# Kernel optimization log

Hardware: AMD Instinct MI355X
Metric: run time of the kernel (lower is better)

Reference implementation:

```python
import jax, jax.numpy as jnp
import numpy as np

B, S, D, H = 1, 4096, 1024, 16
HD = D // H  # head_size = 64

def setup_inputs() -> dict:
    key = jax.random.key(0)
    ks = jax.random.split(key, 9)
    scale = 1.0 / np.sqrt(D)
    return {
        "x": jax.random.normal(ks[0], (B, S, D), jnp.float32),
        "Wq": jax.random.normal(ks[1], (D, D), jnp.float32) * scale,
        "bq": jax.random.normal(ks[2], (D,), jnp.float32) * 0.01,
        "Wk": jax.random.normal(ks[3], (D, D), jnp.float32) * scale,
        "bk": jax.random.normal(ks[4], (D,), jnp.float32) * 0.01,
        "Wv": jax.random.normal(ks[5], (D, D), jnp.float32) * scale,
        "bv": jax.random.normal(ks[6], (D,), jnp.float32) * 0.01,
        "Wo": jax.random.normal(ks[7], (D, D), jnp.float32) * scale,
        "bo": jax.random.normal(ks[8], (D,), jnp.float32) * 0.01,
    }

def _split_heads(t):
    # (B, S, D) -> (B, H, S, HD)
    return t.reshape(B, S, H, HD).transpose(0, 2, 1, 3)

def reference(x, Wq, bq, Wk, bk, Wv, bv, Wo, bo):
    q = _split_heads(x @ Wq + bq)
    k = _split_heads(x @ Wk + bk)
    v = _split_heads(x @ Wv + bv)
    # scores: (B, H, S, S), materialized as in the original naive attention
    scores = jnp.einsum('bhqd,bhkd->bhqk', q, k) / jnp.sqrt(jnp.asarray(HD, q.dtype))
    causal = jnp.tril(jnp.ones((S, S), dtype=bool))  # tril mask, broadcast over (B, H)
    scores = jnp.where(causal[None, None], scores, jnp.asarray(-1e9, scores.dtype))
    attn = jax.nn.softmax(scores, axis=-1)
    out = jnp.einsum('bhqk,bhkd->bhqd', attn, v)  # (B, H, S, HD)
    out = out.transpose(0, 2, 1, 3).reshape(B, S, D)  # combine heads
    return out @ Wo + bo
```

## Files before the change

kernel.cpp:

```cpp
#include <hip/hip_runtime.h>

#define SEQ 4096
#define DM  1024
#define NH  16
#define HDIM 64

typedef unsigned short u16;
typedef unsigned int   u32;
typedef __bf16 bf16x8 __attribute__((ext_vector_type(8)));
typedef float f32x4 __attribute__((ext_vector_type(4)));

__device__ __forceinline__ float bf2f(u16 u) {
    unsigned v = ((unsigned)u) << 16;
    float f;
    __builtin_memcpy(&f, &v, 4);
    return f;
}
__device__ __forceinline__ u16 f2bf(float f) {
    unsigned u;
    __builtin_memcpy(&u, &f, 4);
    return (u16)((u + 0x7fffu + ((u >> 16) & 1u)) >> 16);
}
__device__ __forceinline__ u32 bfpack(float a, float b) {
    u32 ua, ub;
    __builtin_memcpy(&ua, &a, 4);
    __builtin_memcpy(&ub, &b, 4);
    return ((ua + 0x8000u) >> 16) | ((ub + 0x8000u) & 0xffff0000u);
}

typedef const __attribute__((address_space(1))) unsigned int gas_uint;
typedef __attribute__((address_space(3))) unsigned int las_uint;
__device__ __forceinline__ void gld16(const u16* g, u16* l) {
    __builtin_amdgcn_global_load_lds((gas_uint*)g, (las_uint*)l, 16, 0, 0);
}

__device__ __forceinline__ f32x4 mfma16(bf16x8 a, bf16x8 b, f32x4 c) {
    return __builtin_amdgcn_mfma_f32_16x16x32_bf16(a, b, c, 0, 0, 0);
}

#define QSCALE 0.18033688011f

__global__ __launch_bounds__(256) void detect_k(const u16* __restrict__ w,
                                                int* __restrict__ flags) {
    __shared__ float red[256];
    const int t = threadIdx.x;
    float mx = 0.f;
    for (int i = t; i < 4096; i += 256) {
        float v = fabsf(bf2f(w[i]));
        if (v < 3e38f) mx = fmaxf(mx, v);
    }
    red[t] = mx;
    __syncthreads();
    for (int s = 128; s > 0; s >>= 1) {
        if (t < s) red[t] = fmaxf(red[t], red[t + s]);
        __syncthreads();
    }
    if (t == 0) {
        flags[0] = (red[0] > 1e4f) ? 1 : 0;
        flags[1] = 0;
    }
}

__global__ __launch_bounds__(256) void prep_w(const void* w0, const void* w1,
                                              const void* w2, const void* w3,
                                              const void* b0, const void* b1,
                                              const void* b2, const void* b3,
                                              u16* __restrict__ wt,
                                              u16* __restrict__ b_dst,
                                              const int* __restrict__ flags) {
    __shared__ u16 tile[32][33];
    const int f = flags[0];
    const int z = blockIdx.z;
    const void* win[4] = {w0, w1, w2, w3};
    const void* bin[4] = {b0, b1, b2, b3};
    const void* in = win[z];
    u16* out = wt + (size_t)z * DM * DM;
    const float scale = (z == 0) ? QSCALE : 1.0f;

    const int bx = blockIdx.x * 32;
    const int by = blockIdx.y * 32;
    const int tx = threadIdx.x & 31;
    const int ty = threadIdx.x >> 5;
#pragma unroll
    for (int i = ty; i < 32; i += 8) {
        size_t idx = (size_t)(by + i) * DM + bx + tx;
        float v = f ? ((const float*)in)[idx] : bf2f(((const u16*)in)[idx]);
        tile[i][tx] = f2bf(v * scale);
    }
    __syncthreads();
#pragma unroll
    for (int i = ty; i < 32; i += 8) out[(size_t)(bx + i) * DM + by + tx] = tile[tx][i];

    if (blockIdx.x == 0 && blockIdx.y == 0) {
        const void* bi = bin[z];
        for (int i = threadIdx.x; i < DM; i += 256) {
            float v = f ? ((const float*)bi)[i] : bf2f(((const u16*)bi)[i]);
            b_dst[z * DM + i] = f2bf(v * scale);
        }
    }
}

__global__ __launch_bounds__(256) void cvt_x8(const void* __restrict__ src,
                                              u16* __restrict__ dst,
                                              const int* __restrict__ flags) {
    const size_t i = ((size_t)blockIdx.x * 256 + threadIdx.x) * 8;
    if (flags[0]) {
        const float4* s4 = (const float4*)((const float*)src + i);
        float4 a = s4[0], b = s4[1];
        uint4 o;
        o.x = bfpack(a.x, a.y);
        o.y = bfpack(a.z, a.w);
        o.z = bfpack(b.x, b.y);
        o.w = bfpack(b.z, b.w);
        *(uint4*)(dst + i) = o;
    } else {
        *(uint4*)(dst + i) = *(const uint4*)((const u16*)src + i);
    }
}

__global__ __launch_bounds__(256, 2) void gemm128(const u16* __restrict__ A,
                                                  const u16* __restrict__ Bt,
                                                  const u16* __restrict__ bias,
                                                  void* __restrict__ C0,
                                                  void* __restrict__ C1,
                                                  void* __restrict__ C2,
                                                  int M, int N, int K,
                                                  const int* __restrict__ flags) {
    __shared__ u16 As[128 * 32];
    __shared__ u16 Bs[128 * 32];
    const int f    = flags[0];
    const int tid  = threadIdx.x;
    const int lane = tid & 63;
    const int w    = tid >> 6;
    const int m    = lane & 15;
    const int quad = lane >> 4;
    const int wr   = w >> 1;
    const int wc   = w & 1;
    const int mb = blockIdx.x * 128;
    const int nb = blockIdx.y * 128;
    const int mat = nb >> 10;
    const int lnb = nb & 1023;
    void* C = (mat == 0) ? C0 : ((mat == 1) ? C1 : C2);

    f32x4 acc[4][4] = {};

    for (int kb = 0; kb < K; kb += 32) {
        __syncthreads();
#pragma unroll
        for (int i = 0; i < 2; ++i) {
            const int Lb = i * 256 + w * 64;
            const int L  = Lb + lane;
            const int row = L >> 2, cb = L & 3;
            gld16(&A[(size_t)(mb + row) * K + kb + cb * 8], &As[Lb * 8]);
            gld16(&Bt[(size_t)(nb + row) * K + kb + cb * 8], &Bs[Lb * 8]);
        }
        __syncthreads();

        bf16x8 af[4];
#pragma unroll
        for (int mt = 0; mt < 4; ++mt)
            af[mt] = *(const bf16x8*)&As[(wr * 64 + mt * 16 + m) * 32 + quad * 8];
#pragma unroll
        for (int ct = 0; ct < 4; ++ct) {
            bf16x8 bfr = *(const bf16x8*)&Bs[(wc * 64 + ct * 16 + m) * 32 + quad * 8];
#pragma unroll
            for (int mt = 0; mt < 4; ++mt)
                acc[mt][ct] = mfma16(af[mt], bfr, acc[mt][ct]);
        }
    }

#pragma unroll
    for (int ct = 0; ct < 4; ++ct) {
        float bv = bf2f(bias[nb + wc * 64 + ct * 16 + m]);
#pragma unroll
        for (int mt = 0; mt < 4; ++mt) {
#pragma unroll
            for (int r = 0; r < 4; ++r) {
                int row = mb + wr * 64 + mt * 16 + quad * 4 + r;
                size_t idx = (size_t)row * DM + lnb + wc * 64 + ct * 16 + m;
                float v = acc[mt][ct][r] + bv;
                if (f) ((float*)C)[idx] = v;
                else   ((u16*)C)[idx]   = f2bf(v);
            }
        }
    }
}

__global__ __launch_bounds__(256, 2) void gemm_n64(const u16* __restrict__ A,
                                                   const u16* __restrict__ Bt,
                                                   const u16* __restrict__ bias,
                                                   void* __restrict__ C,
                                                   int M, int N, int K,
                                                   const int* __restrict__ flags) {
    __shared__ u16 As[128 * 32];
    __shared__ u16 Bs[64 * 32];
    const int f    = flags[0];
    const int tid  = threadIdx.x;
    const int lane = tid & 63;
    const int w    = tid >> 6;
    const int m    = lane & 15;
    const int quad = lane >> 4;
    const int mb = blockIdx.x * 128;
    const int nb = blockIdx.y * 64;

    f32x4 acc[2][4] = {};

    for (int kb = 0; kb < K; kb += 32) {
        __syncthreads();
#pragma unroll
        for (int i = 0; i < 2; ++i) {
            const int Lb = (2 * w + i) * 64;
            const int L  = Lb + lane;
            const int row = L >> 2, cb = L & 3;
            gld16(&A[(size_t)(mb + row) * K + kb + cb * 8], &As[Lb * 8]);
        }
        {
            const int L = w * 64 + lane;
            const int row = L >> 2, cb = L & 3;
            gld16(&Bt[(size_t)(nb + row) * K + kb + cb * 8], &Bs[w * 512]);
        }
        __syncthreads();

        bf16x8 af[2];
#pragma unroll
        for (int mt = 0; mt < 2; ++mt)
            af[mt] = *(const bf16x8*)&As[(w * 32 + mt * 16 + m) * 32 + quad * 8];
#pragma unroll
        for (int ct = 0; ct < 4; ++ct) {
            bf16x8 bfr = *(const bf16x8*)&Bs[(ct * 16 + m) * 32 + quad * 8];
#pragma unroll
            for (int mt = 0; mt < 2; ++mt)
                acc[mt][ct] = mfma16(af[mt], bfr, acc[mt][ct]);
        }
    }

#pragma unroll
    for (int ct = 0; ct < 4; ++ct) {
        float bv = bf2f(bias[nb + ct * 16 + m]);
#pragma unroll
        for (int mt = 0; mt < 2; ++mt) {
#pragma unroll
            for (int r = 0; r < 4; ++r) {
                int row = mb + w * 32 + mt * 16 + quad * 4 + r;
                size_t idx = (size_t)row * N + nb + ct * 16 + m;
                float v = acc[mt][ct][r] + bv;
                if (f) ((float*)C)[idx] = v;
                else   ((u16*)C)[idx]   = f2bf(v);
            }
        }
    }
}

__global__ __launch_bounds__(256) void vt_k(const u16* __restrict__ V,
                                            u16* __restrict__ Vt) {
    __shared__ u16 T[64][72];
    const int st = blockIdx.x;
    const int h  = blockIdx.y;
    const int t  = threadIdx.x;
    const int sl = t >> 2, c = t & 3;
    const u16* src = &V[(size_t)(st * 64 + sl) * DM + h * 64 + c * 16];
    *(uint4*)&T[sl][c * 16]     = *(const uint4*)src;
    *(uint4*)&T[sl][c * 16 + 8] = *(const uint4*)(src + 8);
    __syncthreads();
    const int dl = t >> 2, c2 = t & 3;
    u16 tmp[16];
#pragma unroll
    for (int i = 0; i < 16; ++i) tmp[i] = T[c2 * 16 + i][dl];
    u16* dst = &Vt[(size_t)(h * 64 + dl) * SEQ + st * 64 + c2 * 16];
    *(uint4*)dst       = *(const uint4*)&tmp[0];
    *(uint4*)(dst + 8) = *(const uint4*)&tmp[8];
}

__global__ __launch_bounds__(256, 2) void attn_split(const u16* __restrict__ Qb,
                                                     const u16* __restrict__ Kb,
                                                     const u16* __restrict__ Vt,
                                                     u16* __restrict__ slot0,
                                                     u16* __restrict__ slot1,
                                                     u16* __restrict__ slot2,
                                                     float* __restrict__ l0,
                                                     float* __restrict__ l1,
                                                     float* __restrict__ l2) {
    __shared__ u16 Ks[2][128 * 64];
    __shared__ u16 Vs[2][64 * 128];

    const int tid  = threadIdx.x;
    const int lane = tid & 63;
    const int w    = tid >> 6;
    const int m    = lane & 15;
    const int quad = lane >> 4;
    const int l3   = lane >> 3;
    const int l4   = lane >> 4;
    const int m7   = m & 7;
    const int cxk  = ((lane & 7) ^ l3) * 8;

    const int b    = blockIdx.x;
    const int x    = b & 7;
    const int u    = b >> 3;
    const int qt2  = 15 - (u / 6);
    const int v6   = u % 6;
    const int head = 2 * x + (v6 / 3);
    const int part = v6 % 3;
    const int hc   = head * HDIM;
    const int n128 = 2 * qt2 + 2;
    const int k0t  = part * n128 / 3;
    const int k1t  = (part + 1) * n128 / 3 - 1;

    const int qw = qt2 * 256 + w * 64;
    const int dw = qw >> 6;

    bf16x8 qf[4][2];
#pragma unroll
    for (int qt4 = 0; qt4 < 4; ++qt4)
#pragma unroll
        for (int c = 0; c < 2; ++c)
            qf[qt4][c] = *(const bf16x8*)&Qb[(size_t)(qw + qt4 * 16 + m) * DM + hc + c * 32 + quad * 8];

    f32x4 o_acc[4][4] = {};
    float l_part[4] = {0.f, 0.f, 0.f, 0.f};

#pragma unroll
    for (int i = 0; i < 4; ++i) {
        const int kr = w * 32 + i * 8 + l3;
        gld16(&Kb[(size_t)(k0t * 128 + kr) * DM + hc + cxk], &Ks[0][(w * 32 + i * 8) * 64]);
        const int vr = w * 16 + i * 4 + l4;
        const int cxv = ((lane & 15) ^ ((i * 4 + l4) & 7)) * 8;
        gld16(&Vt[(size_t)(hc + vr) * SEQ + k0t * 128 + cxv], &Vs[0][(w * 16 + i * 4) * 128]);
    }

    for (int kt = k0t; kt <= k1t; ++kt) {
        const int cur = (kt - k0t) & 1;
        __syncthreads();

        if (kt < k1t) {
            const int nbf = 1 - cur;
            const int nkt = kt + 1;
#pragma unroll
            for (int i = 0; i < 4; ++i) {
                const int kr = w * 32 + i * 8 + l3;
                gld16(&Kb[(size_t)(nkt * 128 + kr) * DM + hc + cxk], &Ks[nbf][(w * 32 + i * 8) * 64]);
                const int vr = w * 16 + i * 4 + l4;
                const int cxv = ((lane & 15) ^ ((i * 4 + l4) & 7)) * 8;
                gld16(&Vt[(size_t)(hc + vr) * SEQ + nkt * 128 + cxv], &Vs[nbf][(w * 16 + i * 4) * 128]);
            }
        }

        const u16* ksb = Ks[cur];
        const u16* vsb = Vs[cur];

#pragma unroll
        for (int h = 0; h < 2; ++h) {
            const int t64 = kt * 2 + h;
            if (t64 > dw) continue;

#pragma unroll
            for (int p = 0; p < 2; ++p) {
                const int ph = 2 * h + p;
                uint4 pa_raw[4];

#pragma unroll
                for (int stt = 0; stt < 2; ++stt) {
                    const int st = ph * 2 + stt;
                    bf16x8 kf[2];
#pragma unroll
                    for (int c = 0; c < 2; ++c)
                        kf[c] = *(const bf16x8*)&ksb[(st * 16 + m) * 64 + (((c * 4 + quad) ^ m7) * 8)];

                    f32x4 sc[4];
#pragma unroll
                    for (int qt4 = 0; qt4 < 4; ++qt4) {
                        f32x4 a = {};
                        a = mfma16(kf[0], qf[qt4][0], a);
                        a = mfma16(kf[1], qf[qt4][1], a);
                        sc[qt4] = a;
                    }

                    if (t64 == dw) {
                        const int stl = 2 * p + stt;
#pragma unroll
                        for (int qt4 = 0; qt4 < 4; ++qt4)
#pragma unroll
                            for (int r = 0; r < 4; ++r) {
                                float pp = __builtin_amdgcn_exp2f(sc[qt4][r]);
                                sc[qt4][r] = (stl * 16 + quad * 4 + r > qt4 * 16 + m) ? 0.f : pp;
                            }
                    } else {
#pragma unroll
                        for (int qt4 = 0; qt4 < 4; ++qt4)
#pragma unroll
                            for (int r = 0; r < 4; ++r)
                                sc[qt4][r] = __builtin_amdgcn_exp2f(sc[qt4][r]);
                    }

#pragma unroll
                    for (int qt4 = 0; qt4 < 4; ++qt4) {
                        l_part[qt4] += sc[qt4][0] + sc[qt4][1] + sc[qt4][2] + sc[qt4][3];
                        const u32 pk0 = bfpack(sc[qt4][0], sc[qt4][1]);
                        const u32 pk1 = bfpack(sc[qt4][2], sc[qt4][3]);
                        if (stt == 0) { pa_raw[qt4].x = pk0; pa_raw[qt4].y = pk1; }
                        else          { pa_raw[qt4].z = pk0; pa_raw[qt4].w = pk1; }
                    }
                }

                bf16x8 pa[4];
#pragma unroll
                for (int qt4 = 0; qt4 < 4; ++qt4) __builtin_memcpy(&pa[qt4], &pa_raw[qt4], 16);

#pragma unroll
                for (int dt = 0; dt < 4; ++dt) {
                    const int base = (dt * 16 + m) * 128;
                    const int clo = ((4 * ph + (quad >> 1)) ^ m7) * 8 + (quad & 1) * 4;
                    const int chi = ((4 * ph + 2 + (quad >> 1)) ^ m7) * 8 + (quad & 1) * 4;
                    uint2 vlo = *(const uint2*)&vsb[base + clo];
                    uint2 vhi = *(const uint2*)&vsb[base + chi];
                    uint4 t;
                    t.x = vlo.x; t.y = vlo.y; t.z = vhi.x; t.w = vhi.y;
                    bf16x8 vf;
                    __builtin_memcpy(&vf, &t, 16);
#pragma unroll
                    for (int qt4 = 0; qt4 < 4; ++qt4)
                        o_acc[qt4][dt] = mfma16(pa[qt4], vf, o_acc[qt4][dt]);
                }
            }
        }
    }

#pragma unroll
    for (int qt4 = 0; qt4 < 4; ++qt4) {
        l_part[qt4] += __shfl_xor(l_part[qt4], 16, 64);
        l_part[qt4] += __shfl_xor(l_part[qt4], 32, 64);
    }

    u16*   dst = (part == 0) ? slot0 : ((part == 1) ? slot1 : slot2);
    float* lb  = (part == 0) ? l0 : ((part == 1) ? l1 : l2);
#pragma unroll
    for (int qt4 = 0; qt4 < 4; ++qt4)
#pragma unroll
        for (int dt = 0; dt < 4; ++dt)
#pragma unroll
            for (int r = 0; r < 4; ++r) {
                int row = qw + qt4 * 16 + quad * 4 + r;
                dst[(size_t)row * DM + hc + dt * 16 + m] = f2bf(o_acc[qt4][dt][r]);
            }
    if (lane < 16) {
#pragma unroll
        for (int qt4 = 0; qt4 < 4; ++qt4)
            lb[head * SEQ + qw + qt4 * 16 + lane] = l_part[qt4];
    }
}

__global__ __launch_bounds__(256) void merge_k(u16* __restrict__ s0,
                                               const u16* __restrict__ s1,
                                               const u16* __restrict__ s2,
                                               const float* __restrict__ l0,
                                               const float* __restrict__ l1,
                                               const float* __restrict__ l2) {
    const int gid = blockIdx.x * 256 + threadIdx.x;
    const int rl = gid >> 7;
    const int cg = gid & 127;
    const int h  = cg >> 3;
    const float inv = 1.0f / (l0[h * SEQ + rl] + l1[h * SEQ + rl] + l2[h * SEQ + rl]);
    uint4 va = *(const uint4*)(s0 + (size_t)rl * DM + cg * 8);
    uint4 vb = *(const uint4*)(s1 + (size_t)rl * DM + cg * 8);
    uint4 vc = *(const uint4*)(s2 + (size_t)rl * DM + cg * 8);
    const u16* a16 = (const u16*)&va;
    const u16* b16 = (const u16*)&vb;
    const u16* c16 = (const u16*)&vc;
    u16 oo[8];
#pragma unroll
    for (int i = 0; i < 8; ++i)
        oo[i] = f2bf((bf2f(a16[i]) + bf2f(b16[i]) + bf2f(c16[i])) * inv);
    *(uint4*)(s0 + (size_t)rl * DM + cg * 8) = *(const uint4*)&oo[0];
}

extern "C" void kernel_launch(void* const* d_in, const int* in_sizes, int n_in,
                              void* d_out, int out_size, void* d_ws, size_t ws_size,
                              hipStream_t stream) {
    (void)in_sizes; (void)n_in; (void)out_size; (void)ws_size;

    u16* ws    = (u16*)d_ws;
    int* flags = (int*)d_ws;
    u16* xc    = ws + 64;
    u16* Vt_g  = xc;
    u16* Wtqkv = xc + (size_t)SEQ * DM;
    u16* Wto   = Wtqkv + (size_t)3 * DM * DM;
    u16* bqkv  = Wto + (size_t)DM * DM;
    u16* boc   = bqkv + 3 * DM;
    u16* Qb    = boc + DM;
    u16* Kb    = Qb + (size_t)SEQ * DM;
    u16* Vb    = Kb + (size_t)SEQ * DM;
    u16* ab    = Vb + (size_t)SEQ * DM;
    u16* slotB = ab + (size_t)SEQ * DM;
    u16* slotC = Vb;
    float* l0f = (float*)Wtqkv;
    float* l1f = l0f + NH * SEQ;
    float* l2f = l1f + NH * SEQ;

    detect_k<<<1, 256, 0, stream>>>((const u16*)d_in[1], flags);

    prep_w<<<dim3(DM / 32, DM / 32, 4), 256, 0, stream>>>(
        d_in[1], d_in[3], d_in[5], d_in[7],
        d_in[2], d_in[4], d_in[6], d_in[8],
        Wtqkv, bqkv, flags);

    cvt_x8<<<SEQ * DM / 2048, 256, 0, stream>>>(d_in[0], xc, flags);

    gemm128<<<dim3(SEQ / 128, 3 * DM / 128), 256, 0, stream>>>(
        xc, Wtqkv, bqkv, Qb, Kb, Vb, SEQ, 3 * DM, DM, flags + 1);

    vt_k<<<dim3(SEQ / 64, NH), 256, 0, stream>>>(Vb, Vt_g);

    attn_split<<<dim3(768), 256, 0, stream>>>(Qb, Kb, Vt_g, ab, slotB, slotC,
                                              l0f, l1f, l2f);

    merge_k<<<dim3(SEQ * 128 / 256), 256, 0, stream>>>(ab, slotB, slotC, l0f, l1f, l2f);

    gemm_n64<<<dim3(SEQ / 128, DM / 64), 256, 0, stream>>>(
        ab, Wto, boc, d_out, SEQ, DM, DM, flags);
}
```

Baseline: 220.5 us.

## Fuse prep kernels, write V transposed from QKV GEMM, remap GEMM block order

Merges the dtype-detect, weight transpose and x conversion kernels into one launch, with each block doing its own dtype check. The QKV GEMM now writes V directly in transposed layout, so the separate transpose kernel and its round trip through global memory go away. Both GEMMs switch to a 1D grid with a remapped block order, likely aiming for better L2 reuse of the weight tiles. This cuts launch count and memory traffic, but adds redundant detection reads in every prep block and uses strided 8-byte stores for the transposed V.

```diff
diff --git a/kernel.cpp b/kernel.cpp
--- a/kernel.cpp
+++ b/kernel.cpp
@@ -40,47 +40,66 @@
 
 #define QSCALE 0.18033688011f
 
-__global__ __launch_bounds__(256) void detect_k(const u16* __restrict__ w,
+__device__ __forceinline__ int self_detect(const void* in, int tid, int* sflag) {
+    if (tid == 0) *sflag = 0;
+    __syncthreads();
+    const u16* p = (const u16*)in;
+    int loc = 0;
+    for (int i = tid; i < 4096; i += 256) {
+        float v = fabsf(bf2f(p[i]));
+        if (v < 3e38f && v > 1e4f) loc = 1;
+    }
+    if (loc) *sflag = 1;
+    __syncthreads();
+    return *sflag;
+}
+
+__global__ __launch_bounds__(256) void prep_all(const void* w0, const void* w1,
+                                                const void* w2, const void* w3,
+                                                const void* b0, const void* b1,
+                                                const void* b2, const void* b3,
+                                                const void* xin,
+                                                u16* __restrict__ wt,
+                                                u16* __restrict__ b_dst,
+                                                u16* __restrict__ xc,
                                                 int* __restrict__ flags) {
-    __shared__ float red[256];
-    const int t = threadIdx.x;
-    float mx = 0.f;
-    for (int i = t; i < 4096; i += 256) {
-        float v = fabsf(bf2f(w[i]));
-        if (v < 3e38f) mx = fmaxf(mx, v);
-    }
-    red[t] = mx;
-    __syncthreads();
-    for (int s = 128; s > 0; s >>= 1) {
-        if (t < s) red[t] = fmaxf(red[t], red[t + s]);
-        __syncthreads();
-    }
-    if (t == 0) {
-        flags[0] = (red[0] > 1e4f) ? 1 : 0;
-        flags[1] = 0;
-    }
-}
-
-__global__ __launch_bounds__(256) void prep_w(const void* w0, const void* w1,
-                                              const void* w2, const void* w3,
-                                              const void* b0, const void* b1,
-                                              const void* b2, const void* b3,
-                                              u16* __restrict__ wt,
-                                              u16* __restrict__ b_dst,
-                                              const int* __restrict__ flags) {
+    __shared__ int sflag;
     __shared__ u16 tile[32][33];
-    const int f = flags[0];
-    const int z = blockIdx.z;
-    const void* win[4] = {w0, w1, w2, w3};
-    const void* bin[4] = {b0, b1, b2, b3};
-    const void* in = win[z];
+    const int z   = blockIdx.z;
+    const int tid = threadIdx.x;
+    const void* srcs[5] = {w0, w1, w2, w3, xin};
+    const void* in = srcs[z];
+    const int f = self_detect(in, tid, &sflag);
+
+    if (z == 4) {
+        const int p = blockIdx.y * 32 + blockIdx.x;
+        if (p == 0 && tid == 0) flags[0] = f;
+#pragma unroll
+        for (int c = 0; c < 2; ++c) {
+            const size_t i = (size_t)p * 4096 + c * 2048 + tid * 8;
+            if (f) {
+                const float4* s4 = (const float4*)((const float*)in + i);
+                float4 a = s4[0], bq = s4[1];
+                uint4 o;
+                o.x = bfpack(a.x, a.y);
+                o.y = bfpack(a.z, a.w);
+                o.z = bfpack(bq.x, bq.y);
+                o.w = bfpack(bq.z, bq.w);
+                *(uint4*)(xc + i) = o;
+            } else {
+                *(uint4*)(xc + i) = *(const uint4*)((const u16*)in + i);
+            }
+        }
+        return;
+    }
+
+    const void* bins[4] = {b0, b1, b2, b3};
     u16* out = wt + (size_t)z * DM * DM;
     const float scale = (z == 0) ? QSCALE : 1.0f;
-
     const int bx = blockIdx.x * 32;
     const int by = blockIdx.y * 32;
-    const int tx = threadIdx.x & 31;
-    const int ty = threadIdx.x >> 5;
+    const int tx = tid & 31;
+    const int ty = tid >> 5;
 #pragma unroll
     for (int i = ty; i < 32; i += 8) {
         size_t idx = (size_t)(by + i) * DM + bx + tx;
@@ -92,43 +111,22 @@
     for (int i = ty; i < 32; i += 8) out[(size_t)(bx + i) * DM + by + tx] = tile[tx][i];
 
     if (blockIdx.x == 0 && blockIdx.y == 0) {
-        const void* bi = bin[z];
-        for (int i = threadIdx.x; i < DM; i += 256) {
+        const void* bi = bins[z];
+        for (int i = tid; i < DM; i += 256) {
             float v = f ? ((const float*)bi)[i] : bf2f(((const u16*)bi)[i]);
             b_dst[z * DM + i] = f2bf(v * scale);
         }
     }
 }
 
-__global__ __launch_bounds__(256) void cvt_x8(const void* __restrict__ src,
-                                              u16* __restrict__ dst,
-                                              const int* __restrict__ flags) {
-    const size_t i = ((size_t)blockIdx.x * 256 + threadIdx.x) * 8;
-    if (flags[0]) {
-        const float4* s4 = (const float4*)((const float*)src + i);
-        float4 a = s4[0], b = s4[1];
-        uint4 o;
-        o.x = bfpack(a.x, a.y);
-        o.y = bfpack(a.z, a.w);
-        o.z = bfpack(b.x, b.y);
-        o.w = bfpack(b.z, b.w);
-        *(uint4*)(dst + i) = o;
-    } else {
-        *(uint4*)(dst + i) = *(const uint4*)((const u16*)src + i);
-    }
-}
-
-__global__ __launch_bounds__(256, 2) void gemm128(const u16* __restrict__ A,
-                                                  const u16* __restrict__ Bt,
-                                                  const u16* __restrict__ bias,
-                                                  void* __restrict__ C0,
-                                                  void* __restrict__ C1,
-                                                  void* __restrict__ C2,
-                                                  int M, int N, int K,
-                                                  const int* __restrict__ flags) {
+__global__ __launch_bounds__(256, 2) void gemm_qkv(const u16* __restrict__ A,
+                                                   const u16* __restrict__ Bt,
+                                                   const u16* __restrict__ bias,
+                                                   u16* __restrict__ Qo,
+                                                   u16* __restrict__ Ko,
+                                                   u16* __restrict__ VtO) {
     __shared__ u16 As[128 * 32];
     __shared__ u16 Bs[128 * 32];
-    const int f    = flags[0];
     const int tid  = threadIdx.x;
     const int lane = tid & 63;
     const int w    = tid >> 6;
@@ -136,23 +134,26 @@
     const int quad = lane >> 4;
     const int wr   = w >> 1;
     const int wc   = w & 1;
-    const int mb = blockIdx.x * 128;
-    const int nb = blockIdx.y * 128;
+
+    const int b   = blockIdx.x;
+    const int x   = b & 7;
+    const int j   = b >> 3;
+    const int nb  = (x * 3 + j % 3) * 128;
+    const int mb  = (j / 3) * 128;
     const int mat = nb >> 10;
     const int lnb = nb & 1023;
-    void* C = (mat == 0) ? C0 : ((mat == 1) ? C1 : C2);
 
     f32x4 acc[4][4] = {};
 
-    for (int kb = 0; kb < K; kb += 32) {
+    for (int kb = 0; kb < DM; kb += 32) {
         __syncthreads();
 #pragma unroll
         for (int i = 0; i < 2; ++i) {
             const int Lb = i * 256 + w * 64;
             const int L  = Lb + lane;
             const int row = L >> 2, cb = L & 3;
-            gld16(&A[(size_t)(mb + row) * K + kb + cb * 8], &As[Lb * 8]);
-            gld16(&Bt[(size_t)(nb + row) * K + kb + cb * 8], &Bs[Lb * 8]);
+            gld16(&A[(size_t)(mb + row) * DM + kb + cb * 8], &As[Lb * 8]);
+            gld16(&Bt[(size_t)(nb + row) * DM + kb + cb * 8], &Bs[Lb * 8]);
         }
         __syncthreads();
 
@@ -169,18 +170,32 @@
         }
     }
 
-#pragma unroll
-    for (int ct = 0; ct < 4; ++ct) {
-        float bv = bf2f(bias[nb + wc * 64 + ct * 16 + m]);
-#pragma unroll
-        for (int mt = 0; mt < 4; ++mt) {
-#pragma unroll
-            for (int r = 0; r < 4; ++r) {
-                int row = mb + wr * 64 + mt * 16 + quad * 4 + r;
-                size_t idx = (size_t)row * DM + lnb + wc * 64 + ct * 16 + m;
-                float v = acc[mt][ct][r] + bv;
-                if (f) ((float*)C)[idx] = v;
-                else   ((u16*)C)[idx]   = f2bf(v);
+    if (mat < 2) {
+        u16* C = mat ? Ko : Qo;
+#pragma unroll
+        for (int ct = 0; ct < 4; ++ct) {
+            float bv = bf2f(bias[nb + wc * 64 + ct * 16 + m]);
+#pragma unroll
+            for (int mt = 0; mt < 4; ++mt)
+#pragma unroll
+                for (int r = 0; r < 4; ++r) {
+                    int row = mb + wr * 64 + mt * 16 + quad * 4 + r;
+                    C[(size_t)row * DM + lnb + wc * 64 + ct * 16 + m] =
+                        f2bf(acc[mt][ct][r] + bv);
+                }
+        }
+    } else {
+#pragma unroll
+        for (int ct = 0; ct < 4; ++ct) {
+            const int n = lnb + wc * 64 + ct * 16 + m;
+            float bv = bf2f(bias[nb + wc * 64 + ct * 16 + m]);
+#pragma unroll
+            for (int mt = 0; mt < 4; ++mt) {
+                const int rowb = mb + wr * 64 + mt * 16 + quad * 4;
+                uint2 pk;
+                pk.x = bfpack(acc[mt][ct][0] + bv, acc[mt][ct][1] + bv);
+                pk.y = bfpack(acc[mt][ct][2] + bv, acc[mt][ct][3] + bv);
+                *(uint2*)&VtO[(size_t)n * SEQ + rowb] = pk;
             }
         }
     }
@@ -190,7 +205,6 @@
                                                    const u16* __restrict__ Bt,
                                                    const u16* __restrict__ bias,
                                                    void* __restrict__ C,
-                                                   int M, int N, int K,
                                                    const int* __restrict__ flags) {
     __shared__ u16 As[128 * 32];
     __shared__ u16 Bs[64 * 32];
@@ -200,24 +214,28 @@
     const int w    = tid >> 6;
     const int m    = lane & 15;
     const int quad = lane >> 4;
-    const int mb = blockIdx.x * 128;
-    const int nb = blockIdx.y * 64;
+
+    const int b  = blockIdx.x;
+    const int x  = b & 7;
+    const int j  = b >> 3;
+    const int nb = (x * 2 + (j & 1)) * 64;
+    const int mb = (j >> 1) * 128;
 
     f32x4 acc[2][4] = {};
 
-    for (int kb = 0; kb < K; kb += 32) {
+    for (int kb = 0; kb < DM; kb += 32) {
         __syncthreads();
 #pragma unroll
         for (int i = 0; i < 2; ++i) {
             const int Lb = (2 * w + i) * 64;
             const int L  = Lb + lane;
             const int row = L >> 2, cb = L & 3;
-            gld16(&A[(size_t)(mb + row) * K + kb + cb * 8], &As[Lb * 8]);
+            gld16(&A[(size_t)(mb + row) * DM + kb + cb * 8], &As[Lb * 8]);
         }
         {
             const int L = w * 64 + lane;
             const int row = L >> 2, cb = L & 3;
-            gld16(&Bt[(size_t)(nb + row) * K + kb + cb * 8], &Bs[w * 512]);
+            gld16(&Bt[(size_t)(nb + row) * DM + kb + cb * 8], &Bs[w * 512]);
         }
         __syncthreads();
 
@@ -242,33 +260,13 @@
 #pragma unroll
             for (int r = 0; r < 4; ++r) {
                 int row = mb + w * 32 + mt * 16 + quad * 4 + r;
-                size_t idx = (size_t)row * N + nb + ct * 16 + m;
+                size_t idx = (size_t)row * DM + nb + ct * 16 + m;
                 float v = acc[mt][ct][r] + bv;
                 if (f) ((float*)C)[idx] = v;
                 else   ((u16*)C)[idx]   = f2bf(v);
             }
         }
     }
-}
-
-__global__ __launch_bounds__(256) void vt_k(const u16* __restrict__ V,
-                                            u16* __restrict__ Vt) {
-    __shared__ u16 T[64][72];
-    const int st = blockIdx.x;
-    const int h  = blockIdx.y;
-    const int t  = threadIdx.x;
-    const int sl = t >> 2, c = t & 3;
-    const u16* src = &V[(size_t)(st * 64 + sl) * DM + h * 64 + c * 16];
-    *(uint4*)&T[sl][c * 16]     = *(const uint4*)src;
-    *(uint4*)&T[sl][c * 16 + 8] = *(const uint4*)(src + 8);
-    __syncthreads();
-    const int dl = t >> 2, c2 = t & 3;
-    u16 tmp[16];
-#pragma unroll
-    for (int i = 0; i < 16; ++i) tmp[i] = T[c2 * 16 + i][dl];
-    u16* dst = &Vt[(size_t)(h * 64 + dl) * SEQ + st * 64 + c2 * 16];
-    *(uint4*)dst       = *(const uint4*)&tmp[0];
-    *(uint4*)(dst + 8) = *(const uint4*)&tmp[8];
 }
 
 __global__ __launch_bounds__(256, 2) void attn_split(const u16* __restrict__ Qb,
@@ -480,40 +478,31 @@
     u16* ws    = (u16*)d_ws;
     int* flags = (int*)d_ws;
     u16* xc    = ws + 64;
-    u16* Vt_g  = xc;
     u16* Wtqkv = xc + (size_t)SEQ * DM;
     u16* Wto   = Wtqkv + (size_t)3 * DM * DM;
     u16* bqkv  = Wto + (size_t)DM * DM;
     u16* boc   = bqkv + 3 * DM;
     u16* Qb    = boc + DM;
     u16* Kb    = Qb + (size_t)SEQ * DM;
-    u16* Vb    = Kb + (size_t)SEQ * DM;
-    u16* ab    = Vb + (size_t)SEQ * DM;
+    u16* Vt_g  = Kb + (size_t)SEQ * DM;
+    u16* ab    = Vt_g + (size_t)SEQ * DM;
     u16* slotB = ab + (size_t)SEQ * DM;
-    u16* slotC = Vb;
+    u16* slotC = xc;
     float* l0f = (float*)Wtqkv;
     float* l1f = l0f + NH * SEQ;
     float* l2f = l1f + NH * SEQ;
 
-    detect_k<<<1, 256, 0, stream>>>((const u16*)d_in[1], flags);
-
-    prep_w<<<dim3(DM / 32, DM / 32, 4), 256, 0, stream>>>(
+    prep_all<<<dim3(32, 32, 5), 256, 0, stream>>>(
         d_in[1], d_in[3], d_in[5], d_in[7],
         d_in[2], d_in[4], d_in[6], d_in[8],
-        Wtqkv, bqkv, flags);
-
-    cvt_x8<<<SEQ * DM / 2048, 256, 0, stream>>>(d_in[0], xc, flags);
-
-    gemm128<<<dim3(SEQ / 128, 3 * DM / 128), 256, 0, stream>>>(
-        xc, Wtqkv, bqkv, Qb, Kb, Vb, SEQ, 3 * DM, DM, flags + 1);
-
-    vt_k<<<dim3(SEQ / 64, NH), 256, 0, stream>>>(Vb, Vt_g);
+        d_in[0], Wtqkv, bqkv, xc, flags);
+
+    gemm_qkv<<<dim3(768), 256, 0, stream>>>(xc, Wtqkv, bqkv, Qb, Kb, Vt_g);
 
     attn_split<<<dim3(768), 256, 0, stream>>>(Qb, Kb, Vt_g, ab, slotB, slotC,
                                               l0f, l1f, l2f);
 
     merge_k<<<dim3(SEQ * 128 / 256), 256, 0, stream>>>(ab, slotB, slotC, l0f, l1f, l2f);
 
-    gemm_n64<<<dim3(SEQ / 128, DM / 64), 256, 0, stream>>>(
-        ab, Wto, boc, d_out, SEQ, DM, DM, flags);
-}
+    gemm_n64<<<dim3(512), 256, 0, stream>>>(ab, Wto, boc, d_out, flags);
+}
```

Result: no change. 224.4 us (+1.8%).
